# Performance work log

Hardware: AMD Instinct MI355X
Metric: run time of the kernel (lower is better)

The kernel has to match this reference:

```python
import jax, jax.numpy as jnp
import numpy as np

N_EMBD = 1024
N_HEAD = 16
HEAD_DIM = N_EMBD // N_HEAD


def setup_inputs() -> dict:
    key = jax.random.key(0)
    ks = jax.random.split(key, 5)
    B, T, C = 4, 2048, N_EMBD
    x = jax.random.normal(ks[0], (B, T, C), dtype=jnp.float32)
    # torch Linear: y = x @ W.T + b; store W in [out, in] like torch
    scale = 1.0 / np.sqrt(C)
    W_attn = jax.random.normal(ks[1], (3 * C, C), dtype=jnp.float32) * scale
    b_attn = jnp.zeros((3 * C,), dtype=jnp.float32)
    W_proj = jax.random.normal(ks[2], (C, C), dtype=jnp.float32) * scale
    b_proj = jnp.zeros((C,), dtype=jnp.float32)
    return {"x": x, "W_attn": W_attn, "b_attn": b_attn, "W_proj": W_proj, "b_proj": b_proj}


def reference(x, W_attn, b_attn, W_proj, b_proj):
    B, T, C = x.shape
    H, D = N_HEAD, HEAD_DIM
    qkv = x @ W_attn.T + b_attn                    # [B,T,3C]
    q, k, v = jnp.split(qkv, 3, axis=-1)
    q = q.reshape(B, T, H, D).transpose(0, 2, 1, 3)  # [B,H,T,D]
    k = k.reshape(B, T, H, D).transpose(0, 2, 1, 3)
    v = v.reshape(B, T, H, D).transpose(0, 2, 1, 3)
    att = jnp.einsum('bhtd,bhsd->bhts', q, k) / jnp.sqrt(jnp.float32(D))  # [B,H,T,T]
    causal = jnp.tril(jnp.ones((T, T), dtype=bool))
    att = jnp.where(causal[None, None], att, -jnp.inf)
    att = jax.nn.softmax(att, axis=-1)
    # dropout is identity in eval mode (pdrop=0.0)
    y = jnp.einsum('bhts,bhsd->bhtd', att, v)      # [B,H,T,D]
    y = y.transpose(0, 2, 1, 3).reshape(B, T, C)
    return y @ W_proj.T + b_proj
```

## Files before the change

kernel.cpp:

```cpp
#include <hip/hip_runtime.h>
#include <stdint.h>


#define SEQ 2048
#define NBATCH 4
#define CEMB 1024
#define NHEAD 16
#define DHEAD 64
#define BTROWS (NBATCH * SEQ)

typedef __bf16 bf16x8 __attribute__((ext_vector_type(8)));
typedef float f32x4 __attribute__((ext_vector_type(4)));
typedef float f32x16 __attribute__((ext_vector_type(16)));
typedef uint32_t u32x4 __attribute__((ext_vector_type(4)));
typedef unsigned short u16;

__device__ __forceinline__ u16 f2bf(float f) {
  union { float f; uint32_t u; } x; x.f = f;
  uint32_t u = x.u;
  return (u16)((u + 0x7FFFu + ((u >> 16) & 1u)) >> 16);
}

__device__ __forceinline__ uint32_t pk2(float a, float b) {
  union { __bf16 h[2]; uint32_t u; } z;
  z.h[0] = (__bf16)a; z.h[1] = (__bf16)b;
  return z.u;
}

__device__ __forceinline__ void gload_lds16(const void* g, void* l) {
  __builtin_amdgcn_global_load_lds(
      (const __attribute__((address_space(1))) uint32_t*)g,
      (__attribute__((address_space(3))) uint32_t*)l, 16, 0, 0);
}

__global__ __launch_bounds__(256) void cvt_f32_bf16_kernel(
    const float* __restrict__ in, u16* __restrict__ out, int n4) {
  int i = blockIdx.x * blockDim.x + threadIdx.x;
  int stride = gridDim.x * blockDim.x;
  for (; i < n4; i += stride) {
    float4 v = reinterpret_cast<const float4*>(in)[i];
    ushort4 o;
    o.x = f2bf(v.x); o.y = f2bf(v.y); o.z = f2bf(v.z); o.w = f2bf(v.w);
    reinterpret_cast<ushort4*>(out)[i] = o;
  }
}

template <bool OUT_BF16>
__global__ __launch_bounds__(256) void gemm_bt_kernel(
    const u16* __restrict__ A, const u16* __restrict__ Bt,
    const float* __restrict__ bias, void* __restrict__ Cout,
    int M, int N, int K) {
  __shared__ u16 As[128][64];
  __shared__ u16 Bs[128][64];
  const int tid = threadIdx.x;
  const int lane = tid & 63;
  const int wave = tid >> 6;
  const int wr = wave >> 1, wc = wave & 1;
  const int m0 = blockIdx.y * 128;
  const int n0 = blockIdx.x * 128;
  const int l15 = lane & 15, lhi = lane >> 4;

  f32x4 acc[4][4];
#pragma unroll
  for (int i = 0; i < 4; i++)
#pragma unroll
    for (int j = 0; j < 4; j++) acc[i][j] = (f32x4){0.f, 0.f, 0.f, 0.f};

  const int srow = lane >> 3;
  const int scol = (lane & 7) * 8;

  for (int kt = 0; kt < K; kt += 64) {
#pragma unroll
    for (int i = 0; i < 4; i++) {
      int rr = (wave * 4 + i) * 8 + srow;
      gload_lds16(A + (size_t)(m0 + rr) * K + kt + scol, &As[(wave * 4 + i) * 8][0]);
      gload_lds16(Bt + (size_t)(n0 + rr) * K + kt + scol, &Bs[(wave * 4 + i) * 8][0]);
    }
    __syncthreads();
#pragma unroll
    for (int ks = 0; ks < 2; ks++) {
      bf16x8 af[4], bfr[4];
#pragma unroll
      for (int mi = 0; mi < 4; mi++)
        af[mi] = *(const bf16x8*)&As[wr * 64 + mi * 16 + l15][ks * 32 + lhi * 8];
#pragma unroll
      for (int ni = 0; ni < 4; ni++)
        bfr[ni] = *(const bf16x8*)&Bs[wc * 64 + ni * 16 + l15][ks * 32 + lhi * 8];
#pragma unroll
      for (int mi = 0; mi < 4; mi++)
#pragma unroll
        for (int ni = 0; ni < 4; ni++)
          acc[mi][ni] = __builtin_amdgcn_mfma_f32_16x16x32_bf16(
              af[mi], bfr[ni], acc[mi][ni], 0, 0, 0);
    }
    __syncthreads();
  }

#pragma unroll
  for (int mi = 0; mi < 4; mi++) {
#pragma unroll
    for (int ni = 0; ni < 4; ni++) {
      int n = n0 + wc * 64 + ni * 16 + l15;
      float bv = bias[n];
#pragma unroll
      for (int r = 0; r < 4; r++) {
        int m = m0 + wr * 64 + mi * 16 + lhi * 4 + r;
        float v = acc[mi][ni][r] + bv;
        if constexpr (OUT_BF16)
          ((u16*)Cout)[(size_t)m * N + n] = f2bf(v);
        else
          ((float*)Cout)[(size_t)m * N + n] = v;
      }
    }
  }
}

__global__ __launch_bounds__(256) void attn_kernel(
    const u16* __restrict__ qkv, u16* __restrict__ yatt) {
  __shared__ u16 Ks[128][64];
  __shared__ u16 Vt[64][132];

  const int tid = threadIdx.x;
  const int lane = tid & 63;
  const int wave = tid >> 6;
  const int p = blockIdx.x;
  const int bh = blockIdx.y;
  const int b = bh >> 4, h = bh & 15;
  const int l31 = lane & 31, hi = lane >> 5;

  const size_t rs = 3 * CEMB;
  const u16* qb = qkv + (size_t)b * SEQ * rs + h * DHEAD;
  const u16* kb = qb + CEMB;
  const u16* vb = qb + 2 * CEMB;

  const float SCLL2E = 0.125f * 1.44269504088896f;

  for (int pass = 0; pass < 2; ++pass) {
    const int qt = pass ? (15 - p) : p;
    const int q0 = qt * 128;
    const int qabs = q0 + wave * 32 + l31;

    bf16x8 qf[4];
    {
      const u16* qp = qb + (size_t)qabs * rs + hi * 8;
#pragma unroll
      for (int dc = 0; dc < 4; dc++) qf[dc] = *(const bf16x8*)(qp + dc * 16);
    }

    float m_acc = -1e30f, l_acc = 0.f;
    f32x16 o_acc[2];
    o_acc[0] = (f32x16)(0.f);
    o_acc[1] = (f32x16)(0.f);

    for (int s0 = 0; s0 <= q0; s0 += 128) {
#pragma unroll
      for (int c = 0; c < 4; c++) {
        int row0 = (c * 4 + wave) * 8;
        int row = row0 + (lane >> 3);
        int cb = (lane & 7) ^ (row & 7);
        gload_lds16(kb + (size_t)(s0 + row) * rs + cb * 8, &Ks[row0][0]);
      }
#pragma unroll
      for (int half = 0; half < 2; ++half) {
        const u16* gv = vb + (size_t)(s0 + half * 64 + lane) * rs + wave * 16;
        union { u32x4 q[2]; u16 u[16]; } tv;
        tv.q[0] = *(const u32x4*)gv;
        tv.q[1] = *(const u32x4*)(gv + 8);
#pragma unroll
        for (int j = 0; j < 16; j++) Vt[wave * 16 + j][half * 64 + lane] = tv.u[j];
      }
      __syncthreads();

      f32x16 sf[4];
      __builtin_amdgcn_s_setprio(1);
#pragma unroll
      for (int kt = 0; kt < 4; kt++) {
        f32x16 s = (f32x16)(0.f);
        int key = kt * 32 + l31;
#pragma unroll
        for (int dc = 0; dc < 4; dc++) {
          int cb = (dc * 2 + hi) ^ (key & 7);
          const bf16x8 kf = *(const bf16x8*)((const u16*)&Ks[key][0] + cb * 8);
          s = __builtin_amdgcn_mfma_f32_32x32x16_bf16(kf, qf[dc], s, 0, 0, 0);
        }
        sf[kt] = s;
      }
      __builtin_amdgcn_s_setprio(0);

      if (s0 == q0) {
#pragma unroll
        for (int kt = 0; kt < 4; kt++)
#pragma unroll
          for (int r = 0; r < 16; r++) {
            int key = s0 + kt * 32 + (r & 3) + 8 * (r >> 2) + 4 * hi;
            if (key > qabs) sf[kt][r] = -3e38f;
          }
      }

      float t16[16];
#pragma unroll
      for (int i = 0; i < 16; i++)
        t16[i] = fmaxf(fmaxf(sf[0][i], sf[1][i]), fmaxf(sf[2][i], sf[3][i]));
#pragma unroll
      for (int i = 0; i < 8; i++) t16[i] = fmaxf(t16[i], t16[i + 8]);
#pragma unroll
      for (int i = 0; i < 4; i++) t16[i] = fmaxf(t16[i], t16[i + 4]);
      float cmax = fmaxf(fmaxf(t16[0], t16[1]), fmaxf(t16[2], t16[3]));
      cmax = fmaxf(cmax, __shfl_xor(cmax, 32, 64));

      if (!__all(cmax <= m_acc + 64.0f)) {
        float mnew = fmaxf(m_acc, cmax);
        float scf = __builtin_amdgcn_exp2f((m_acc - mnew) * SCLL2E);
        m_acc = mnew;
        l_acc *= scf;
        float scr[16];
#pragma unroll
        for (int r = 0; r < 16; r++)
          scr[r] = __shfl(scf, (r & 3) + 8 * (r >> 2) + 4 * hi, 64);
#pragma unroll
        for (int r = 0; r < 16; r++) {
          o_acc[0][r] *= scr[r];
          o_acc[1][r] *= scr[r];
        }
      }

      const float c1 = -m_acc * SCLL2E;
#pragma unroll
      for (int kt = 0; kt < 4; kt++)
#pragma unroll
        for (int r = 0; r < 16; r++)
          sf[kt][r] = __builtin_amdgcn_exp2f(fmaf(sf[kt][r], SCLL2E, c1));
#pragma unroll
      for (int i = 0; i < 16; i++)
        t16[i] = (sf[0][i] + sf[1][i]) + (sf[2][i] + sf[3][i]);
#pragma unroll
      for (int i = 0; i < 8; i++) t16[i] = t16[i] + t16[i + 8];
#pragma unroll
      for (int i = 0; i < 4; i++) t16[i] = t16[i] + t16[i + 4];
      float ps = (t16[0] + t16[1]) + (t16[2] + t16[3]);
      ps += __shfl_xor(ps, 32, 64);
      l_acc += ps;

      bf16x8 pa[8];
#pragma unroll
      for (int ks = 0; ks < 8; ks++) {
        const int t = ks >> 1;
        const int ra = (ks & 1) * 8;
        uint32_t a  = pk2(sf[t][ra + 0], sf[t][ra + 1]);
        uint32_t b2 = pk2(sf[t][ra + 2], sf[t][ra + 3]);
        uint32_t cc = pk2(sf[t][ra + 4], sf[t][ra + 5]);
        uint32_t dd = pk2(sf[t][ra + 6], sf[t][ra + 7]);
        uint32_t snd0 = hi ? a : cc;
        uint32_t snd1 = hi ? b2 : dd;
        uint32_t r0 = __shfl_xor(snd0, 32, 64);
        uint32_t r1 = __shfl_xor(snd1, 32, 64);
        union { bf16x8 v; uint32_t w[4]; } u;
        u.w[0] = hi ? r0 : a;
        u.w[1] = hi ? r1 : b2;
        u.w[2] = hi ? cc : r0;
        u.w[3] = hi ? dd : r1;
        pa[ks] = u.v;
      }

      __builtin_amdgcn_s_setprio(1);
#pragma unroll
      for (int dt = 0; dt < 2; dt++) {
        const u16* vrow = &Vt[dt * 32 + l31][hi * 8];
#pragma unroll
        for (int ks = 0; ks < 8; ks++) {
          union { bf16x8 v; uint2 d[2]; } u;
          u.d[0] = *(const uint2*)(vrow + ks * 16);
          u.d[1] = *(const uint2*)(vrow + ks * 16 + 4);
          o_acc[dt] = __builtin_amdgcn_mfma_f32_32x32x16_bf16(pa[ks], u.v, o_acc[dt], 0, 0, 0);
        }
      }
      __builtin_amdgcn_s_setprio(0);
      __syncthreads();
    }

    float rl = 1.0f / l_acc;
#pragma unroll
    for (int r = 0; r < 16; r++) {
      int crow = (r & 3) + 8 * (r >> 2) + 4 * hi;
      float linv = __shfl(rl, crow, 64);
      int t = q0 + wave * 32 + crow;
      u16* yp = yatt + ((size_t)(b * SEQ + t)) * CEMB + h * DHEAD + l31;
      yp[0]  = f2bf(o_acc[0][r] * linv);
      yp[32] = f2bf(o_acc[1][r] * linv);
    }
  }
}

extern "C" void kernel_launch(void* const* d_in, const int* in_sizes, int n_in,
                              void* d_out, int out_size, void* d_ws, size_t ws_size,
                              hipStream_t stream) {
  const float* x      = (const float*)d_in[0];
  const float* W_attn = (const float*)d_in[1];
  const float* b_attn = (const float*)d_in[2];
  const float* W_proj = (const float*)d_in[3];
  const float* b_proj = (const float*)d_in[4];
  float* out = (float*)d_out;

  u16* Xb   = (u16*)d_ws;
  u16* Wab  = Xb  + (size_t)BTROWS * CEMB;
  u16* Wpb  = Wab + (size_t)3 * CEMB * CEMB;
  u16* QKV  = Wpb + (size_t)CEMB * CEMB;
  u16* Yatt = QKV + (size_t)BTROWS * 3 * CEMB;

  cvt_f32_bf16_kernel<<<2048, 256, 0, stream>>>(x, Xb, BTROWS * CEMB / 4);
  cvt_f32_bf16_kernel<<<1024, 256, 0, stream>>>(W_attn, Wab, 3 * CEMB * CEMB / 4);
  cvt_f32_bf16_kernel<<<512, 256, 0, stream>>>(W_proj, Wpb, CEMB * CEMB / 4);

  gemm_bt_kernel<true><<<dim3(3 * CEMB / 128, BTROWS / 128), 256, 0, stream>>>(
      Xb, Wab, b_attn, QKV, BTROWS, 3 * CEMB, CEMB);

  attn_kernel<<<dim3(8, NBATCH * NHEAD), 256, 0, stream>>>(QKV, Yatt);

  gemm_bt_kernel<false><<<dim3(CEMB / 128, BTROWS / 128), 256, 0, stream>>>(
      Yatt, Wpb, b_proj, out, BTROWS, CEMB, CEMB);
}
```

Measured before the change: 331.1 us.

## Double-buffer K/V tiles in attention to prefetch next chunk during compute

Attention K and V shared-memory tiles become double-buffered. The next chunk's K goes to LDS asynchronously and its V is held in registers while the current chunk's QK^T and softmax run, and V is written transposed to the spare buffer before the PV MFMAs. This removes one barrier per iteration and hides global-load latency behind compute. In exchange it doubles LDS use, which may reduce occupancy, and adds register pressure from the held V values.

```diff
diff --git a/kernel.cpp b/kernel.cpp
--- a/kernel.cpp
+++ b/kernel.cpp
@@ -117,8 +117,8 @@
 
 __global__ __launch_bounds__(256) void attn_kernel(
     const u16* __restrict__ qkv, u16* __restrict__ yatt) {
-  __shared__ u16 Ks[128][64];
-  __shared__ u16 Vt[64][132];
+  __shared__ u16 Ks[2][128][64];
+  __shared__ u16 Vt[2][64][132];
 
   const int tid = threadIdx.x;
   const int lane = tid & 63;
@@ -135,10 +135,13 @@
 
   const float SCLL2E = 0.125f * 1.44269504088896f;
 
+  u32x4 tva, tvb2, tvc, tvd;
+
   for (int pass = 0; pass < 2; ++pass) {
     const int qt = pass ? (15 - p) : p;
     const int q0 = qt * 128;
     const int qabs = q0 + wave * 32 + l31;
+    const int nchunk = qt + 1;
 
     bf16x8 qf[4];
     {
@@ -152,24 +155,53 @@
     o_acc[0] = (f32x16)(0.f);
     o_acc[1] = (f32x16)(0.f);
 
-    for (int s0 = 0; s0 <= q0; s0 += 128) {
+    {
+      const u16* gv0 = vb + (size_t)(0 + lane) * rs + wave * 16;
+      const u16* gv1 = vb + (size_t)(64 + lane) * rs + wave * 16;
+      tva = *(const u32x4*)gv0; tvb2 = *(const u32x4*)(gv0 + 8);
+      tvc = *(const u32x4*)gv1; tvd = *(const u32x4*)(gv1 + 8);
 #pragma unroll
       for (int c = 0; c < 4; c++) {
         int row0 = (c * 4 + wave) * 8;
         int row = row0 + (lane >> 3);
         int cb = (lane & 7) ^ (row & 7);
-        gload_lds16(kb + (size_t)(s0 + row) * rs + cb * 8, &Ks[row0][0]);
-      }
-#pragma unroll
-      for (int half = 0; half < 2; ++half) {
-        const u16* gv = vb + (size_t)(s0 + half * 64 + lane) * rs + wave * 16;
-        union { u32x4 q[2]; u16 u[16]; } tv;
-        tv.q[0] = *(const u32x4*)gv;
-        tv.q[1] = *(const u32x4*)(gv + 8);
-#pragma unroll
-        for (int j = 0; j < 16; j++) Vt[wave * 16 + j][half * 64 + lane] = tv.u[j];
-      }
-      __syncthreads();
+        gload_lds16(kb + (size_t)row * rs + cb * 8, &Ks[0][row0][0]);
+      }
+      union { u32x4 q; u16 u[8]; } x;
+      x.q = tva;
+#pragma unroll
+      for (int j = 0; j < 8; j++) Vt[0][wave * 16 + j][lane] = x.u[j];
+      x.q = tvb2;
+#pragma unroll
+      for (int j = 0; j < 8; j++) Vt[0][wave * 16 + 8 + j][lane] = x.u[j];
+      x.q = tvc;
+#pragma unroll
+      for (int j = 0; j < 8; j++) Vt[0][wave * 16 + j][64 + lane] = x.u[j];
+      x.q = tvd;
+#pragma unroll
+      for (int j = 0; j < 8; j++) Vt[0][wave * 16 + 8 + j][64 + lane] = x.u[j];
+    }
+    __syncthreads();
+
+    for (int ci = 0; ci < nchunk; ci++) {
+      const int cur = ci & 1;
+      const int nxt = cur ^ 1;
+      const bool pre = (ci + 1 < nchunk);
+
+      if (pre) {
+        const int s1 = (ci + 1) * 128;
+        const u16* gv0 = vb + (size_t)(s1 + lane) * rs + wave * 16;
+        const u16* gv1 = vb + (size_t)(s1 + 64 + lane) * rs + wave * 16;
+        tva = *(const u32x4*)gv0; tvb2 = *(const u32x4*)(gv0 + 8);
+        tvc = *(const u32x4*)gv1; tvd = *(const u32x4*)(gv1 + 8);
+#pragma unroll
+        for (int c = 0; c < 4; c++) {
+          int row0 = (c * 4 + wave) * 8;
+          int row = row0 + (lane >> 3);
+          int cb = (lane & 7) ^ (row & 7);
+          gload_lds16(kb + (size_t)(s1 + row) * rs + cb * 8, &Ks[nxt][row0][0]);
+        }
+      }
 
       f32x16 sf[4];
       __builtin_amdgcn_s_setprio(1);
@@ -180,14 +212,15 @@
 #pragma unroll
         for (int dc = 0; dc < 4; dc++) {
           int cb = (dc * 2 + hi) ^ (key & 7);
-          const bf16x8 kf = *(const bf16x8*)((const u16*)&Ks[key][0] + cb * 8);
+          const bf16x8 kf = *(const bf16x8*)((const u16*)&Ks[cur][key][0] + cb * 8);
           s = __builtin_amdgcn_mfma_f32_32x32x16_bf16(kf, qf[dc], s, 0, 0, 0);
         }
         sf[kt] = s;
       }
       __builtin_amdgcn_s_setprio(0);
 
-      if (s0 == q0) {
+      if (ci == nchunk - 1) {
+        const int s0 = ci * 128;
 #pragma unroll
         for (int kt = 0; kt < 4; kt++)
 #pragma unroll
@@ -262,10 +295,26 @@
         pa[ks] = u.v;
       }
 
+      if (pre) {
+        union { u32x4 q; u16 u[8]; } x;
+        x.q = tva;
+#pragma unroll
+        for (int j = 0; j < 8; j++) Vt[nxt][wave * 16 + j][lane] = x.u[j];
+        x.q = tvb2;
+#pragma unroll
+        for (int j = 0; j < 8; j++) Vt[nxt][wave * 16 + 8 + j][lane] = x.u[j];
+        x.q = tvc;
+#pragma unroll
+        for (int j = 0; j < 8; j++) Vt[nxt][wave * 16 + j][64 + lane] = x.u[j];
+        x.q = tvd;
+#pragma unroll
+        for (int j = 0; j < 8; j++) Vt[nxt][wave * 16 + 8 + j][64 + lane] = x.u[j];
+      }
+
       __builtin_amdgcn_s_setprio(1);
 #pragma unroll
       for (int dt = 0; dt < 2; dt++) {
-        const u16* vrow = &Vt[dt * 32 + l31][hi * 8];
+        const u16* vrow = &Vt[cur][dt * 32 + l31][hi * 8];
 #pragma unroll
         for (int ks = 0; ks < 8; ks++) {
           union { bf16x8 v; uint2 d[2]; } u;
@@ -275,6 +324,7 @@
         }
       }
       __builtin_amdgcn_s_setprio(0);
+
       __syncthreads();
     }
 
```

After: 340.2 us. 2.8% more time.

## Rewrite GEMMs as 8-wave double-buffered 256-row tiles with swizzled LDS

Applied to the files above, without the earlier changes.

Replaces the 128x128 single-buffered GEMM with a 512-thread kernel using 256xBN tiles and double-buffered LDS. The next K-tile's global-to-LDS loads are issued during the current tile's MFMA phases. An XOR swizzle on LDS columns avoids bank conflicts, and workgroup indices are remapped across XCDs for cache locality. This adds larger LDS usage and more barriers per tile, and the grids shrink (192 and 128 blocks), which may leave CUs underused.

```diff
diff --git a/kernel.cpp b/kernel.cpp
--- a/kernel.cpp
+++ b/kernel.cpp
@@ -45,74 +45,141 @@
   }
 }
 
-template <bool OUT_BF16>
-__global__ __launch_bounds__(256) void gemm_bt_kernel(
+template <int BN, int WROWS, bool OUT_BF16>
+__global__ __launch_bounds__(512, 2) void gemm8p_kernel(
     const u16* __restrict__ A, const u16* __restrict__ Bt,
     const float* __restrict__ bias, void* __restrict__ Cout,
     int M, int N, int K) {
-  __shared__ u16 As[128][64];
-  __shared__ u16 Bs[128][64];
+  constexpr int BM = 256;
+  constexpr int WCOLS = 8 / WROWS;
+  constexpr int WM = BM / WROWS;
+  constexpr int WN = BN / WCOLS;
+  constexpr int MI = WM / 16;
+  constexpr int NI = WN / 16;
+  constexpr int PHASES = MI / 2;
+  constexpr int ACH = BM / 64;
+  constexpr int BCH = BN / 64;
+
+  __shared__ u16 As[2][BM][64];
+  __shared__ u16 Bs[2][BN][64];
+
   const int tid = threadIdx.x;
   const int lane = tid & 63;
   const int wave = tid >> 6;
-  const int wr = wave >> 1, wc = wave & 1;
-  const int m0 = blockIdx.y * 128;
-  const int n0 = blockIdx.x * 128;
+  const int wr = wave / WCOLS, wc = wave % WCOLS;
   const int l15 = lane & 15, lhi = lane >> 4;
 
-  f32x4 acc[4][4];
-#pragma unroll
-  for (int i = 0; i < 4; i++)
-#pragma unroll
-    for (int j = 0; j < 4; j++) acc[i][j] = (f32x4){0.f, 0.f, 0.f, 0.f};
-
-  const int srow = lane >> 3;
-  const int scol = (lane & 7) * 8;
-
-  for (int kt = 0; kt < K; kt += 64) {
-#pragma unroll
-    for (int i = 0; i < 4; i++) {
-      int rr = (wave * 4 + i) * 8 + srow;
-      gload_lds16(A + (size_t)(m0 + rr) * K + kt + scol, &As[(wave * 4 + i) * 8][0]);
-      gload_lds16(Bt + (size_t)(n0 + rr) * K + kt + scol, &Bs[(wave * 4 + i) * 8][0]);
+  const int nbx = gridDim.x;
+  const int nwg = nbx * gridDim.y;
+  const int orig = (int)blockIdx.y * nbx + (int)blockIdx.x;
+  const int swz = (orig & 7) * (nwg >> 3) + (orig >> 3);
+  const int m0 = (swz / nbx) * BM;
+  const int n0 = (swz % nbx) * BN;
+
+  const int grow = tid >> 3;
+  const int gcb = tid & 7;
+
+  f32x4 acc[MI][NI];
+#pragma unroll
+  for (int mi = 0; mi < MI; mi++)
+#pragma unroll
+    for (int ni = 0; ni < NI; ni++) acc[mi][ni] = (f32x4){0.f, 0.f, 0.f, 0.f};
+
+#pragma unroll
+  for (int c = 0; c < ACH; c++) {
+    int row = c * 64 + grow;
+    int cb = gcb ^ (row & 7);
+    gload_lds16(A + (size_t)(m0 + row) * K + cb * 8, &As[0][row][gcb * 8]);
+  }
+#pragma unroll
+  for (int c = 0; c < BCH; c++) {
+    int row = c * 64 + grow;
+    int cb = gcb ^ (row & 7);
+    gload_lds16(Bt + (size_t)(n0 + row) * K + cb * 8, &Bs[0][row][gcb * 8]);
+  }
+  __syncthreads();
+
+  const int NT = K / 64;
+  for (int t = 0; t < NT; t++) {
+    const int cur = t & 1, nxt = cur ^ 1;
+    const bool pre = (t + 1 < NT);
+    const int kt1 = (t + 1) * 64;
+    bf16x8 bfr[NI][2];
+#pragma unroll
+    for (int p = 0; p < PHASES; p++) {
+      if (p == 0) {
+#pragma unroll
+        for (int ni = 0; ni < NI; ni++)
+#pragma unroll
+          for (int ks = 0; ks < 2; ks++) {
+            int row = wc * WN + ni * 16 + l15;
+            int b = ks * 4 + lhi;
+            bfr[ni][ks] = *(const bf16x8*)&Bs[cur][row][(b ^ (row & 7)) * 8];
+          }
+      }
+      bf16x8 af[2][2];
+#pragma unroll
+      for (int i = 0; i < 2; i++)
+#pragma unroll
+        for (int ks = 0; ks < 2; ks++) {
+          int row = wr * WM + (p * 2 + i) * 16 + l15;
+          int b = ks * 4 + lhi;
+          af[i][ks] = *(const bf16x8*)&As[cur][row][(b ^ (row & 7)) * 8];
+        }
+      if (pre && p == 0) {
+#pragma unroll
+        for (int c = 0; c < ACH; c++) {
+          int row = c * 64 + grow;
+          int cb = gcb ^ (row & 7);
+          gload_lds16(A + (size_t)(m0 + row) * K + kt1 + cb * 8,
+                      &As[nxt][row][gcb * 8]);
+        }
+      }
+      if (pre && p == 1) {
+#pragma unroll
+        for (int c = 0; c < BCH; c++) {
+          int row = c * 64 + grow;
+          int cb = gcb ^ (row & 7);
+          gload_lds16(Bt + (size_t)(n0 + row) * K + kt1 + cb * 8,
+                      &Bs[nxt][row][gcb * 8]);
+        }
+      }
+      asm volatile("" ::: "memory");
+      __builtin_amdgcn_s_barrier();
+      __builtin_amdgcn_s_setprio(1);
+#pragma unroll
+      for (int ks = 0; ks < 2; ks++)
+#pragma unroll
+        for (int i = 0; i < 2; i++)
+#pragma unroll
+          for (int ni = 0; ni < NI; ni++)
+            acc[p * 2 + i][ni] = __builtin_amdgcn_mfma_f32_16x16x32_bf16(
+                af[i][ks], bfr[ni][ks], acc[p * 2 + i][ni], 0, 0, 0);
+      __builtin_amdgcn_s_setprio(0);
+      asm volatile("" ::: "memory");
+      __builtin_amdgcn_s_barrier();
     }
     __syncthreads();
-#pragma unroll
-    for (int ks = 0; ks < 2; ks++) {
-      bf16x8 af[4], bfr[4];
-#pragma unroll
-      for (int mi = 0; mi < 4; mi++)
-        af[mi] = *(const bf16x8*)&As[wr * 64 + mi * 16 + l15][ks * 32 + lhi * 8];
-#pragma unroll
-      for (int ni = 0; ni < 4; ni++)
-        bfr[ni] = *(const bf16x8*)&Bs[wc * 64 + ni * 16 + l15][ks * 32 + lhi * 8];
-#pragma unroll
-      for (int mi = 0; mi < 4; mi++)
-#pragma unroll
-        for (int ni = 0; ni < 4; ni++)
-          acc[mi][ni] = __builtin_amdgcn_mfma_f32_16x16x32_bf16(
-              af[mi], bfr[ni], acc[mi][ni], 0, 0, 0);
-    }
-    __syncthreads();
-  }
-
-#pragma unroll
-  for (int mi = 0; mi < 4; mi++) {
-#pragma unroll
-    for (int ni = 0; ni < 4; ni++) {
-      int n = n0 + wc * 64 + ni * 16 + l15;
-      float bv = bias[n];
+  }
+
+  float bv[NI];
+#pragma unroll
+  for (int ni = 0; ni < NI; ni++) bv[ni] = bias[n0 + wc * WN + ni * 16 + l15];
+#pragma unroll
+  for (int mi = 0; mi < MI; mi++)
+#pragma unroll
+    for (int ni = 0; ni < NI; ni++) {
+      int n = n0 + wc * WN + ni * 16 + l15;
 #pragma unroll
       for (int r = 0; r < 4; r++) {
-        int m = m0 + wr * 64 + mi * 16 + lhi * 4 + r;
-        float v = acc[mi][ni][r] + bv;
+        int m = m0 + wr * WM + mi * 16 + lhi * 4 + r;
+        float v = acc[mi][ni][r] + bv[ni];
         if constexpr (OUT_BF16)
           ((u16*)Cout)[(size_t)m * N + n] = f2bf(v);
         else
           ((float*)Cout)[(size_t)m * N + n] = v;
       }
     }
-  }
 }
 
 __global__ __launch_bounds__(256) void attn_kernel(
@@ -311,11 +378,11 @@
   cvt_f32_bf16_kernel<<<1024, 256, 0, stream>>>(W_attn, Wab, 3 * CEMB * CEMB / 4);
   cvt_f32_bf16_kernel<<<512, 256, 0, stream>>>(W_proj, Wpb, CEMB * CEMB / 4);
 
-  gemm_bt_kernel<true><<<dim3(3 * CEMB / 128, BTROWS / 128), 256, 0, stream>>>(
+  gemm8p_kernel<256, 2, true><<<dim3(3 * CEMB / 256, BTROWS / 256), 512, 0, stream>>>(
       Xb, Wab, b_attn, QKV, BTROWS, 3 * CEMB, CEMB);
 
   attn_kernel<<<dim3(8, NBATCH * NHEAD), 256, 0, stream>>>(QKV, Yatt);
 
-  gemm_bt_kernel<false><<<dim3(CEMB / 128, BTROWS / 128), 256, 0, stream>>>(
+  gemm8p_kernel<128, 4, false><<<dim3(CEMB / 128, BTROWS / 256), 512, 0, stream>>>(
       Yatt, Wpb, b_proj, out, BTROWS, CEMB, CEMB);
 }
```

Result: faster. 307.5 us (-7.1%).
